# Kernel tuning notes

Hardware: AMD Instinct MI355X
Metric: run time of the kernel (lower is better)

Reference implementation:

```python
import jax, jax.numpy as jnp
import numpy as np

IN_FEATURES = 512
ACTION_DIM = 32
TRIL_DIM = ACTION_DIM * (ACTION_DIM + 1) // 2  # 528
BATCH = 65536
# Row-major lower-triangular indices; matches torch boolean-mask assignment order.
_ROWS, _COLS = np.tril_indices(ACTION_DIM)


def setup_inputs() -> dict:
    key = jax.random.key(0)
    k1, k2, k3, k4, k5 = jax.random.split(key, 5)
    logits = jax.random.normal(k1, (BATCH, IN_FEATURES), dtype=jnp.float32)
    best_action = jax.random.normal(k2, (BATCH, ACTION_DIM), dtype=jnp.float32)
    actions = jax.random.normal(k3, (BATCH, ACTION_DIM), dtype=jnp.float32)
    W = jax.random.normal(k4, (TRIL_DIM, IN_FEATURES), dtype=jnp.float32) * 0.02
    b = jax.random.normal(k5, (TRIL_DIM,), dtype=jnp.float32) * 0.02
    return {"logits": logits, "best_action": best_action, "actions": actions, "W": W, "b": b}


def reference(logits, best_action, actions, W, b):
    # Linear: [B, in_features] -> [B, tril_dim]
    flat_trils = logits @ W.T + b
    B = logits.shape[0]
    n = ACTION_DIM
    # Scatter flat vector into lower-triangular slots (row-major order).
    mats = jnp.zeros((B, n, n), dtype=flat_trils.dtype).at[:, _ROWS, _COLS].set(flat_trils)
    diag = jnp.eye(n, dtype=flat_trils.dtype)
    # Square the diagonal entries, keep off-diagonal entries as-is.
    tril = mats * mats * diag + (1.0 - diag) * mats
    action_diff = actions - best_action  # [B, n]
    vec = jnp.einsum('bij,bj->bi', tril, action_diff)  # [B, n]
    advantage = -0.5 * jnp.sum(vec * vec, axis=-1, keepdims=True)  # [B, 1]
    return advantage
```

## Files before the change

### kernel.cpp

```cpp
#include <hip/hip_runtime.h>
#include <hip/hip_bf16.h>


typedef __attribute__((ext_vector_type(8))) __bf16 bf16x8;
typedef __attribute__((ext_vector_type(4))) float f32x4;

#define AS1 __attribute__((address_space(1)))
#define AS3 __attribute__((address_space(3)))

__device__ __forceinline__ unsigned short f2b(float x) {
  unsigned u = __builtin_bit_cast(unsigned, x);
  u += 0x7fffu + ((u >> 16) & 1u);
  return (unsigned short)(u >> 16);
}
__device__ __forceinline__ float b2f(unsigned short h) {
  unsigned u = ((unsigned)h) << 16;
  return __builtin_bit_cast(float, u);
}

#define NFRAG 34
#define WK_BYTES (NFRAG * 1024)
#define AOFF (2 * WK_BYTES)
#define ABUF 4096
#define FL_STRIDE 1216
#define PL_OFF (64 * FL_STRIDE)
#define SMEM_BYTES (PL_OFF + 1024)

__global__ void prep_wp(const float* __restrict__ W, unsigned short* __restrict__ WP) {
  int t = blockIdx.x * 256 + threadIdx.x;
  int lane = t & 63;
  int u = t >> 6;
  int nf = u % NFRAG;
  int k16 = u / NFRAG;
  int n = nf * 16 + (lane & 15);
  int k0 = k16 * 32 + (lane >> 4) * 8;
  unsigned short h[8];
  if (n < 528) {
    const float* src = W + (size_t)n * 512 + k0;
#pragma unroll
    for (int j = 0; j < 8; ++j) h[j] = f2b(src[j]);
  } else {
#pragma unroll
    for (int j = 0; j < 8; ++j) h[j] = 0;
  }
  uint4 p;
  p.x = (unsigned)h[0] | ((unsigned)h[1] << 16);
  p.y = (unsigned)h[2] | ((unsigned)h[3] << 16);
  p.z = (unsigned)h[4] | ((unsigned)h[5] << 16);
  p.w = (unsigned)h[6] | ((unsigned)h[7] << 16);
  *(uint4*)(WP + (size_t)t * 8) = p;
}

template <int IT>
__device__ __forceinline__ float epi_partial(const char* smem,
                                             const float* __restrict__ actions,
                                             const float* __restrict__ best,
                                             int brow, int l) {
  float d[32];
  const float* ap = actions + (size_t)(brow + l) * 32;
  const float* bp = best + (size_t)(brow + l) * 32;
#pragma unroll
  for (int q = 0; q < 8; ++q) {
    float4 av = *(const float4*)(ap + q * 4);
    float4 bv = *(const float4*)(bp + q * 4);
    d[q * 4 + 0] = av.x - bv.x;
    d[q * 4 + 1] = av.y - bv.y;
    d[q * 4 + 2] = av.z - bv.z;
    d[q * 4 + 3] = av.w - bv.w;
  }
  const char* frow = smem + l * FL_STRIDE;
  const int swz = (l & 7) << 4;
  float ssum = 0.f;
#pragma unroll
  for (int ii = 0; ii < 8; ++ii) {
    const int i = IT + ii * 4;
    const int tri2 = i * (i + 1);
    const int s0 = tri2 >> 4;
    const int s1 = (tri2 + 2 * i) >> 4;
    float vec = 0.f;
#pragma unroll
    for (int s = s0; s <= s1; ++s) {
      uint4 w = *(const uint4*)(frow + ((s * 16) ^ swz));
      const unsigned* wp = (const unsigned*)&w;
#pragma unroll
      for (int e = 0; e < 8; ++e) {
        const int j = s * 8 + e - (tri2 >> 1);
        if (j < 0 || j > i) continue;
        unsigned short h = (e & 1) ? (unsigned short)(wp[e >> 1] >> 16)
                                   : (unsigned short)(wp[e >> 1] & 0xffffu);
        float v = b2f(h);
        if (j == i) vec += v * v * d[i];
        else        vec += v * d[j];
      }
    }
    ssum += vec * vec;
  }
  return ssum;
}

__global__ void __launch_bounds__(256, 2)
adv_kernel(const float* __restrict__ logits,
           const float* __restrict__ best,
           const float* __restrict__ actions,
           const float* __restrict__ bvec,
           const unsigned short* __restrict__ WP,
           float* __restrict__ out) {
  extern __shared__ char smem[];
  const int tid = threadIdx.x;
  const int l   = tid & 63;
  const int wid = tid >> 6;
  const int lr  = l & 15;
  const int lg  = l >> 4;
  const int start = wid * 8 + (wid > 0 ? 1 : 0);
  const int brow = blockIdx.x * 64;

  f32x4 acc[4][9];
  {
    f32x4 zero = {0.f, 0.f, 0.f, 0.f};
#pragma unroll
    for (int m = 0; m < 4; ++m)
#pragma unroll
      for (int n = 0; n < 9; ++n) acc[m][n] = zero;
  }

  const float* agbase = logits + (size_t)(brow + wid * 16 + lr) * 512 + lg * 8;

#define STAGE_W(dst, ks)                                                        \
  {                                                                             \
    const char* sW = (const char*)WP + (size_t)(ks) * WK_BYTES;                 \
    _Pragma("unroll")                                                           \
    for (int q = 0; q < 8; ++q) {                                               \
      int off = (q * 4 + wid) * 1024;                                           \
      __builtin_amdgcn_global_load_lds((AS1 unsigned int*)(sW + off + l * 16),  \
          (AS3 unsigned int*)((dst) + off), 16, 0, 0);                          \
    }                                                                           \
    if (wid < 2) {                                                              \
      int off = (32 + wid) * 1024;                                              \
      __builtin_amdgcn_global_load_lds((AS1 unsigned int*)(sW + off + l * 16),  \
          (AS3 unsigned int*)((dst) + off), 16, 0, 0);                          \
    }                                                                           \
  }

#define LOAD_A(dst, ks)                                                         \
  {                                                                             \
    const float* g = agbase + (ks) * 32;                                        \
    (dst)[0] = *(const float4*)(g);                                             \
    (dst)[1] = *(const float4*)(g + 4);                                         \
  }

#define WRITE_A(buf_idx, src)                                                   \
  {                                                                             \
    uint4 p;                                                                    \
    p.x = f2b((src)[0].x) | ((unsigned)f2b((src)[0].y) << 16);                  \
    p.y = f2b((src)[0].z) | ((unsigned)f2b((src)[0].w) << 16);                  \
    p.z = f2b((src)[1].x) | ((unsigned)f2b((src)[1].y) << 16);                  \
    p.w = f2b((src)[1].z) | ((unsigned)f2b((src)[1].w) << 16);                  \
    *(uint4*)(smem + AOFF + (buf_idx) * ABUF + tid * 16) = p;                   \
  }

#define COMPUTE(p)                                                              \
  {                                                                             \
    const char* ab = smem + AOFF + (p) * ABUF;                                  \
    const char* wb = smem + (p) * WK_BYTES;                                     \
    bf16x8 a[4];                                                                \
    _Pragma("unroll")                                                           \
    for (int m = 0; m < 4; ++m)                                                 \
      a[m] = *(const bf16x8*)(ab + m * 1024 + l * 16);                          \
    _Pragma("unroll")                                                           \
    for (int n = 0; n < 9; ++n) {                                               \
      bf16x8 w = *(const bf16x8*)(wb + (start + n) * 1024 + l * 16);            \
      _Pragma("unroll")                                                         \
      for (int m = 0; m < 4; ++m)                                               \
        acc[m][n] = __builtin_amdgcn_mfma_f32_16x16x32_bf16(a[m], w, acc[m][n], 0, 0, 0); \
    }                                                                           \
  }

  float4 pf0[2], pf1[2];
  LOAD_A(pf0, 0)
  LOAD_A(pf1, 1)
  STAGE_W(smem, 0)
  WRITE_A(0, pf0)
  __syncthreads();

  for (int t2 = 0; t2 < 16; t2 += 2) {
    if (t2 < 15) STAGE_W(smem + WK_BYTES, t2 + 1)
    if (t2 < 14) LOAD_A(pf0, t2 + 2)
    COMPUTE(0)
    if (t2 < 15) WRITE_A(1, pf1)
    __syncthreads();
    {
      int t = t2 + 1;
      if (t < 15) STAGE_W(smem, t + 1)
      if (t < 14) LOAD_A(pf1, t + 2)
      COMPUTE(1)
      if (t < 15) WRITE_A(0, pf0)
      __syncthreads();
    }
  }

#pragma unroll
  for (int n = 0; n < 9; ++n) {
    int nf = start + n;
    if (nf >= 33) continue;
    int f = nf * 16 + lr;
    float bb = bvec[f];
#pragma unroll
    for (int m = 0; m < 4; ++m)
#pragma unroll
      for (int r = 0; r < 4; ++r) {
        int row = m * 16 + lg * 4 + r;
        int byte = row * FL_STRIDE + ((f * 2) ^ ((row & 7) << 4));
        *(unsigned short*)(smem + byte) = f2b(acc[m][n][r] + bb);
      }
  }
  __syncthreads();

  float ssum;
  switch (wid) {
    case 0:  ssum = epi_partial<0>(smem, actions, best, brow, l); break;
    case 1:  ssum = epi_partial<1>(smem, actions, best, brow, l); break;
    case 2:  ssum = epi_partial<2>(smem, actions, best, brow, l); break;
    default: ssum = epi_partial<3>(smem, actions, best, brow, l); break;
  }
  ((float*)(smem + PL_OFF))[l * 4 + wid] = ssum;
  __syncthreads();
  if (tid < 64) {
    f32x4 p4 = *(const f32x4*)(smem + PL_OFF + tid * 16);
    out[brow + tid] = -0.5f * (p4[0] + p4[1] + p4[2] + p4[3]);
  }
}

extern "C" void kernel_launch(void* const* d_in, const int* in_sizes, int n_in,
                              void* d_out, int out_size, void* d_ws, size_t ws_size,
                              hipStream_t stream) {
  const float* logits  = (const float*)d_in[0];
  const float* best    = (const float*)d_in[1];
  const float* actions = (const float*)d_in[2];
  const float* W       = (const float*)d_in[3];
  const float* bvec    = (const float*)d_in[4];
  float* out = (float*)d_out;
  unsigned short* WP = (unsigned short*)d_ws;

  hipLaunchKernelGGL(prep_wp, dim3(136), dim3(256), 0, stream, W, WP);
  int M = in_sizes[0] / 512;
  hipLaunchKernelGGL(adv_kernel, dim3(M / 64), dim3(256), SMEM_BYTES, stream,
                     logits, best, actions, bvec, WP, out);
}
```

Before: 70.69 us.

## Replace syncthreads with partial vmcnt waits and raw barriers in GEMM pipeline

The main K-loop now uses explicit s_waitcnt with a partial vmcnt and raw s_barrier calls in place of __syncthreads. The intent is to let the next A-tile global loads stay in flight across the barrier while the LDS-direct W loads complete. The W staging is also made uniform: every wave issues 9 loads, and out-of-range slots are clamped to a padded LDS region. Sched barriers pin the order in which loads are issued. The manual vmcnt accounting is fragile: if the count of outstanding loads is wrong, the kernel can read LDS data before it has arrived.

```diff
diff --git a/kernel.cpp b/kernel.cpp
--- a/kernel.cpp
+++ b/kernel.cpp
@@ -20,11 +20,16 @@
 
 #define NFRAG 34
 #define WK_BYTES (NFRAG * 1024)
-#define AOFF (2 * WK_BYTES)
+#define WB_LDS 36864
+#define AOFF (2 * WB_LDS)
 #define ABUF 4096
 #define FL_STRIDE 1216
 #define PL_OFF (64 * FL_STRIDE)
-#define SMEM_BYTES (PL_OFF + 1024)
+#define SMEM_BYTES 81920
+
+#define SBAR0 __builtin_amdgcn_sched_barrier(0);
+#define WAITC(N) asm volatile("s_waitcnt vmcnt(" #N ") lgkmcnt(0)" ::: "memory");
+#define RAWBAR { SBAR0 __builtin_amdgcn_s_barrier(); SBAR0 }
 
 __global__ void prep_wp(const float* __restrict__ W, unsigned short* __restrict__ WP) {
   int t = blockIdx.x * 256 + threadIdx.x;
@@ -129,14 +134,10 @@
   {                                                                             \
     const char* sW = (const char*)WP + (size_t)(ks) * WK_BYTES;                 \
     _Pragma("unroll")                                                           \
-    for (int q = 0; q < 8; ++q) {                                               \
+    for (int q = 0; q < 9; ++q) {                                               \
       int off = (q * 4 + wid) * 1024;                                           \
-      __builtin_amdgcn_global_load_lds((AS1 unsigned int*)(sW + off + l * 16),  \
-          (AS3 unsigned int*)((dst) + off), 16, 0, 0);                          \
-    }                                                                           \
-    if (wid < 2) {                                                              \
-      int off = (32 + wid) * 1024;                                              \
-      __builtin_amdgcn_global_load_lds((AS1 unsigned int*)(sW + off + l * 16),  \
+      int soff = off < WK_BYTES ? off : (WK_BYTES - 1024);                      \
+      __builtin_amdgcn_global_load_lds((AS1 unsigned int*)(sW + soff + l * 16), \
           (AS3 unsigned int*)((dst) + off), 16, 0, 0);                          \
     }                                                                           \
   }
@@ -161,7 +162,7 @@
 #define COMPUTE(p)                                                              \
   {                                                                             \
     const char* ab = smem + AOFF + (p) * ABUF;                                  \
-    const char* wb = smem + (p) * WK_BYTES;                                     \
+    const char* wb = smem + (p) * WB_LDS;                                       \
     bf16x8 a[4];                                                                \
     _Pragma("unroll")                                                           \
     for (int m = 0; m < 4; ++m)                                                 \
@@ -176,27 +177,38 @@
   }
 
   float4 pf0[2], pf1[2];
+  STAGE_W(smem, 0)
+  SBAR0
   LOAD_A(pf0, 0)
   LOAD_A(pf1, 1)
-  STAGE_W(smem, 0)
+  SBAR0
   WRITE_A(0, pf0)
-  __syncthreads();
+  asm volatile("s_waitcnt lgkmcnt(0)" ::: "memory");
+  RAWBAR
 
   for (int t2 = 0; t2 < 16; t2 += 2) {
-    if (t2 < 15) STAGE_W(smem + WK_BYTES, t2 + 1)
+    if (t2 < 15) STAGE_W(smem + WB_LDS, t2 + 1)
+    SBAR0
     if (t2 < 14) LOAD_A(pf0, t2 + 2)
+    SBAR0
     COMPUTE(0)
     if (t2 < 15) WRITE_A(1, pf1)
-    __syncthreads();
+    if (t2 <= 12) { WAITC(2) }
+    else          { WAITC(0) }
+    RAWBAR
     {
-      int t = t2 + 1;
+      const int t = t2 + 1;
       if (t < 15) STAGE_W(smem, t + 1)
+      SBAR0
       if (t < 14) LOAD_A(pf1, t + 2)
+      SBAR0
       COMPUTE(1)
       if (t < 15) WRITE_A(0, pf0)
-      __syncthreads();
+      if (t <= 13) { WAITC(2) RAWBAR }
     }
   }
+  WAITC(0)
+  RAWBAR
 
 #pragma unroll
   for (int n = 0; n < 9; ++n) {
```

New measurement: 72.22 us. 2.2% more time.

## Load GEMM operands straight to registers and double the block to 128 rows

Applied to the files above, without the earlier changes.

The kernel stops staging W and A tiles in LDS with double buffering and barriers. Each wave now loads its own 9 W fragments and 4 A row-fragments from global memory into registers, converts A to bf16 in registers, and runs the MFMAs with raised scheduling priority. Blocks grow to 512 threads covering 128 rows, so two halves share the epilogue LDS. This removes LDS traffic and per-step syncs, but each wave now re-reads W from global/L2 instead of sharing it through LDS. The register prefetch only runs one step ahead, so latency hiding depends on occupancy.

```diff
diff --git a/kernel.cpp b/kernel.cpp
--- a/kernel.cpp
+++ b/kernel.cpp
@@ -4,9 +4,6 @@
 
 typedef __attribute__((ext_vector_type(8))) __bf16 bf16x8;
 typedef __attribute__((ext_vector_type(4))) float f32x4;
-
-#define AS1 __attribute__((address_space(1)))
-#define AS3 __attribute__((address_space(3)))
 
 __device__ __forceinline__ unsigned short f2b(float x) {
   unsigned u = __builtin_bit_cast(unsigned, x);
@@ -20,11 +17,9 @@
 
 #define NFRAG 34
 #define WK_BYTES (NFRAG * 1024)
-#define AOFF (2 * WK_BYTES)
-#define ABUF 4096
 #define FL_STRIDE 1216
-#define PL_OFF (64 * FL_STRIDE)
-#define SMEM_BYTES (PL_OFF + 1024)
+#define PL_OFF (128 * FL_STRIDE)
+#define SMEM_BYTES (PL_OFF + 2048)
 
 __global__ void prep_wp(const float* __restrict__ W, unsigned short* __restrict__ WP) {
   int t = blockIdx.x * 256 + threadIdx.x;
@@ -55,10 +50,10 @@
 __device__ __forceinline__ float epi_partial(const char* smem,
                                              const float* __restrict__ actions,
                                              const float* __restrict__ best,
-                                             int brow, int l) {
+                                             int growg, int lrow) {
   float d[32];
-  const float* ap = actions + (size_t)(brow + l) * 32;
-  const float* bp = best + (size_t)(brow + l) * 32;
+  const float* ap = actions + (size_t)growg * 32;
+  const float* bp = best + (size_t)growg * 32;
 #pragma unroll
   for (int q = 0; q < 8; ++q) {
     float4 av = *(const float4*)(ap + q * 4);
@@ -68,8 +63,8 @@
     d[q * 4 + 2] = av.z - bv.z;
     d[q * 4 + 3] = av.w - bv.w;
   }
-  const char* frow = smem + l * FL_STRIDE;
-  const int swz = (l & 7) << 4;
+  const char* frow = smem + lrow * FL_STRIDE;
+  const int swz = (lrow & 7) << 4;
   float ssum = 0.f;
 #pragma unroll
   for (int ii = 0; ii < 8; ++ii) {
@@ -98,7 +93,7 @@
   return ssum;
 }
 
-__global__ void __launch_bounds__(256, 2)
+__global__ void __launch_bounds__(512, 2)
 adv_kernel(const float* __restrict__ logits,
            const float* __restrict__ best,
            const float* __restrict__ actions,
@@ -106,13 +101,15 @@
            const unsigned short* __restrict__ WP,
            float* __restrict__ out) {
   extern __shared__ char smem[];
-  const int tid = threadIdx.x;
-  const int l   = tid & 63;
-  const int wid = tid >> 6;
-  const int lr  = l & 15;
-  const int lg  = l >> 4;
-  const int start = wid * 8 + (wid > 0 ? 1 : 0);
-  const int brow = blockIdx.x * 64;
+  const int tid  = threadIdx.x;
+  const int l    = tid & 63;
+  const int wid  = tid >> 6;
+  const int half = wid >> 2;
+  const int wc   = wid & 3;
+  const int lr   = l & 15;
+  const int lg   = l >> 4;
+  const int start = wc * 8 + (wc > 0 ? 1 : 0);
+  const int brow = blockIdx.x * 128;
 
   f32x4 acc[4][9];
   {
@@ -123,78 +120,59 @@
       for (int n = 0; n < 9; ++n) acc[m][n] = zero;
   }
 
-  const float* agbase = logits + (size_t)(brow + wid * 16 + lr) * 512 + lg * 8;
-
-#define STAGE_W(dst, ks)                                                        \
+  const char* wlane = (const char*)WP + (size_t)start * 1024 + (size_t)l * 16;
+  const float* ag0 = logits + (size_t)(brow + half * 64 + 0 * 16 + lr) * 512 + lg * 8;
+  const float* ag1 = logits + (size_t)(brow + half * 64 + 1 * 16 + lr) * 512 + lg * 8;
+  const float* ag2 = logits + (size_t)(brow + half * 64 + 2 * 16 + lr) * 512 + lg * 8;
+  const float* ag3 = logits + (size_t)(brow + half * 64 + 3 * 16 + lr) * 512 + lg * 8;
+
+  uint4 wreg[9];
+  float4 araw[4][2];
+
+#define LOADW(t)                                                                \
   {                                                                             \
-    const char* sW = (const char*)WP + (size_t)(ks) * WK_BYTES;                 \
+    const char* p = wlane + (size_t)(t) * WK_BYTES;                             \
     _Pragma("unroll")                                                           \
-    for (int q = 0; q < 8; ++q) {                                               \
-      int off = (q * 4 + wid) * 1024;                                           \
-      __builtin_amdgcn_global_load_lds((AS1 unsigned int*)(sW + off + l * 16),  \
-          (AS3 unsigned int*)((dst) + off), 16, 0, 0);                          \
-    }                                                                           \
-    if (wid < 2) {                                                              \
-      int off = (32 + wid) * 1024;                                              \
-      __builtin_amdgcn_global_load_lds((AS1 unsigned int*)(sW + off + l * 16),  \
-          (AS3 unsigned int*)((dst) + off), 16, 0, 0);                          \
-    }                                                                           \
-  }
-
-#define LOAD_A(dst, ks)                                                         \
+    for (int n = 0; n < 9; ++n) wreg[n] = *(const uint4*)(p + n * 1024);        \
+  }
+#define LOADA(t)                                                                \
   {                                                                             \
-    const float* g = agbase + (ks) * 32;                                        \
-    (dst)[0] = *(const float4*)(g);                                             \
-    (dst)[1] = *(const float4*)(g + 4);                                         \
-  }
-
-#define WRITE_A(buf_idx, src)                                                   \
-  {                                                                             \
-    uint4 p;                                                                    \
-    p.x = f2b((src)[0].x) | ((unsigned)f2b((src)[0].y) << 16);                  \
-    p.y = f2b((src)[0].z) | ((unsigned)f2b((src)[0].w) << 16);                  \
-    p.z = f2b((src)[1].x) | ((unsigned)f2b((src)[1].y) << 16);                  \
-    p.w = f2b((src)[1].z) | ((unsigned)f2b((src)[1].w) << 16);                  \
-    *(uint4*)(smem + AOFF + (buf_idx) * ABUF + tid * 16) = p;                   \
-  }
-
-#define COMPUTE(p)                                                              \
-  {                                                                             \
-    const char* ab = smem + AOFF + (p) * ABUF;                                  \
-    const char* wb = smem + (p) * WK_BYTES;                                     \
-    bf16x8 a[4];                                                                \
-    _Pragma("unroll")                                                           \
-    for (int m = 0; m < 4; ++m)                                                 \
-      a[m] = *(const bf16x8*)(ab + m * 1024 + l * 16);                          \
-    _Pragma("unroll")                                                           \
-    for (int n = 0; n < 9; ++n) {                                               \
-      bf16x8 w = *(const bf16x8*)(wb + (start + n) * 1024 + l * 16);            \
-      _Pragma("unroll")                                                         \
-      for (int m = 0; m < 4; ++m)                                               \
-        acc[m][n] = __builtin_amdgcn_mfma_f32_16x16x32_bf16(a[m], w, acc[m][n], 0, 0, 0); \
-    }                                                                           \
-  }
-
-  float4 pf0[2], pf1[2];
-  LOAD_A(pf0, 0)
-  LOAD_A(pf1, 1)
-  STAGE_W(smem, 0)
-  WRITE_A(0, pf0)
-  __syncthreads();
-
-  for (int t2 = 0; t2 < 16; t2 += 2) {
-    if (t2 < 15) STAGE_W(smem + WK_BYTES, t2 + 1)
-    if (t2 < 14) LOAD_A(pf0, t2 + 2)
-    COMPUTE(0)
-    if (t2 < 15) WRITE_A(1, pf1)
-    __syncthreads();
-    {
-      int t = t2 + 1;
-      if (t < 15) STAGE_W(smem, t + 1)
-      if (t < 14) LOAD_A(pf1, t + 2)
-      COMPUTE(1)
-      if (t < 15) WRITE_A(0, pf0)
-      __syncthreads();
+    araw[0][0] = *(const float4*)(ag0 + (t) * 32);                              \
+    araw[0][1] = *(const float4*)(ag0 + (t) * 32 + 4);                          \
+    araw[1][0] = *(const float4*)(ag1 + (t) * 32);                              \
+    araw[1][1] = *(const float4*)(ag1 + (t) * 32 + 4);                          \
+    araw[2][0] = *(const float4*)(ag2 + (t) * 32);                              \
+    araw[2][1] = *(const float4*)(ag2 + (t) * 32 + 4);                          \
+    araw[3][0] = *(const float4*)(ag3 + (t) * 32);                              \
+    araw[3][1] = *(const float4*)(ag3 + (t) * 32 + 4);                          \
+  }
+
+  LOADW(0)
+  LOADA(0)
+
+  for (int t = 0; t < 16; ++t) {
+    bf16x8 a[4];
+#pragma unroll
+    for (int m = 0; m < 4; ++m) {
+      bf16x8 af;
+      af[0] = (__bf16)araw[m][0].x; af[1] = (__bf16)araw[m][0].y;
+      af[2] = (__bf16)araw[m][0].z; af[3] = (__bf16)araw[m][0].w;
+      af[4] = (__bf16)araw[m][1].x; af[5] = (__bf16)araw[m][1].y;
+      af[6] = (__bf16)araw[m][1].z; af[7] = (__bf16)araw[m][1].w;
+      a[m] = af;
+    }
+    __builtin_amdgcn_s_setprio(1);
+#pragma unroll
+    for (int n = 0; n < 9; ++n) {
+      bf16x8 w = __builtin_bit_cast(bf16x8, wreg[n]);
+#pragma unroll
+      for (int m = 0; m < 4; ++m)
+        acc[m][n] = __builtin_amdgcn_mfma_f32_16x16x32_bf16(a[m], w, acc[m][n], 0, 0, 0);
+    }
+    __builtin_amdgcn_s_setprio(0);
+    if (t < 15) {
+      LOADW(t + 1)
+      LOADA(t + 1)
     }
   }
 
@@ -208,23 +186,27 @@
     for (int m = 0; m < 4; ++m)
 #pragma unroll
       for (int r = 0; r < 4; ++r) {
-        int row = m * 16 + lg * 4 + r;
+        int row = half * 64 + m * 16 + lg * 4 + r;
         int byte = row * FL_STRIDE + ((f * 2) ^ ((row & 7) << 4));
         *(unsigned short*)(smem + byte) = f2b(acc[m][n][r] + bb);
       }
   }
   __syncthreads();
 
-  float ssum;
-  switch (wid) {
-    case 0:  ssum = epi_partial<0>(smem, actions, best, brow, l); break;
-    case 1:  ssum = epi_partial<1>(smem, actions, best, brow, l); break;
-    case 2:  ssum = epi_partial<2>(smem, actions, best, brow, l); break;
-    default: ssum = epi_partial<3>(smem, actions, best, brow, l); break;
-  }
-  ((float*)(smem + PL_OFF))[l * 4 + wid] = ssum;
+  {
+    const int lrow = half * 64 + l;
+    const int growg = brow + lrow;
+    float ssum;
+    switch (wc) {
+      case 0:  ssum = epi_partial<0>(smem, actions, best, growg, lrow); break;
+      case 1:  ssum = epi_partial<1>(smem, actions, best, growg, lrow); break;
+      case 2:  ssum = epi_partial<2>(smem, actions, best, growg, lrow); break;
+      default: ssum = epi_partial<3>(smem, actions, best, growg, lrow); break;
+    }
+    ((float*)(smem + PL_OFF))[lrow * 4 + wc] = ssum;
+  }
   __syncthreads();
-  if (tid < 64) {
+  if (tid < 128) {
     f32x4 p4 = *(const f32x4*)(smem + PL_OFF + tid * 16);
     out[brow + tid] = -0.5f * (p4[0] + p4[1] + p4[2] + p4[3]);
   }
@@ -243,6 +225,6 @@
 
   hipLaunchKernelGGL(prep_wp, dim3(136), dim3(256), 0, stream, W, WP);
   int M = in_sizes[0] / 512;
-  hipLaunchKernelGGL(adv_kernel, dim3(M / 64), dim3(256), SMEM_BYTES, stream,
+  hipLaunchKernelGGL(adv_kernel, dim3(M / 128), dim3(512), SMEM_BYTES, stream,
                      logits, best, actions, bvec, WP, out);
 }
```

Result: slower. 98.08 us (+38.8%).

## Split output columns across two blocks per row tile and reduce partial vectors separately

Applied to the files above, without the earlier changes.

Each 64-row tile is now handled by two blocks, each computing half of the 528 output columns. This halves the per-block W staging and accumulator footprint, which lets occupancy rise from two to three blocks per CU. The logits are now read straight from global memory into registers inside the compute step and converted to bf16, replacing the LDS A staging. Each block writes partial triangular matrix-vector products to a workspace, and a new reduce kernel combines the two halves and computes the squared sum. The cost is that logits are read twice, there is extra workspace traffic, and an additional kernel launch.

```diff
diff --git a/kernel.cpp b/kernel.cpp
--- a/kernel.cpp
+++ b/kernel.cpp
@@ -20,11 +20,10 @@
 
 #define NFRAG 34
 #define WK_BYTES (NFRAG * 1024)
-#define AOFF (2 * WK_BYTES)
-#define ABUF 4096
-#define FL_STRIDE 1216
-#define PL_OFF (64 * FL_STRIDE)
-#define SMEM_BYTES (PL_OFF + 1024)
+#define WSTEP 17408
+#define FL2_STRIDE 640
+#define SMEM_BYTES 40960
+#define WS2_OFF 557056
 
 __global__ void prep_wp(const float* __restrict__ W, unsigned short* __restrict__ WP) {
   int t = blockIdx.x * 256 + threadIdx.x;
@@ -51,14 +50,14 @@
   *(uint4*)(WP + (size_t)t * 8) = p;
 }
 
-template <int IT>
-__device__ __forceinline__ float epi_partial(const char* smem,
+template <int IT, int LO>
+__device__ __forceinline__ void epi_partial2(const char* smem,
                                              const float* __restrict__ actions,
                                              const float* __restrict__ best,
-                                             int brow, int l) {
+                                             int grow, int lrow, float* pv) {
   float d[32];
-  const float* ap = actions + (size_t)(brow + l) * 32;
-  const float* bp = best + (size_t)(brow + l) * 32;
+  const float* ap = actions + (size_t)grow * 32;
+  const float* bp = best + (size_t)grow * 32;
 #pragma unroll
   for (int q = 0; q < 8; ++q) {
     float4 av = *(const float4*)(ap + q * 4);
@@ -68,166 +67,188 @@
     d[q * 4 + 2] = av.z - bv.z;
     d[q * 4 + 3] = av.w - bv.w;
   }
-  const char* frow = smem + l * FL_STRIDE;
-  const int swz = (l & 7) << 4;
-  float ssum = 0.f;
+  const char* frow = smem + lrow * FL2_STRIDE;
+  const int swz = (lrow & 7) << 4;
 #pragma unroll
   for (int ii = 0; ii < 8; ++ii) {
     const int i = IT + ii * 4;
-    const int tri2 = i * (i + 1);
-    const int s0 = tri2 >> 4;
-    const int s1 = (tri2 + 2 * i) >> 4;
+    const int tri = (i * (i + 1)) >> 1;
+    const int jlo = (LO > tri) ? (LO - tri) : 0;
+    const int jhi = (i < LO + 271 - tri) ? i : (LO + 271 - tri);
     float vec = 0.f;
-#pragma unroll
-    for (int s = s0; s <= s1; ++s) {
-      uint4 w = *(const uint4*)(frow + ((s * 16) ^ swz));
-      const unsigned* wp = (const unsigned*)&w;
-#pragma unroll
-      for (int e = 0; e < 8; ++e) {
-        const int j = s * 8 + e - (tri2 >> 1);
-        if (j < 0 || j > i) continue;
-        unsigned short h = (e & 1) ? (unsigned short)(wp[e >> 1] >> 16)
-                                   : (unsigned short)(wp[e >> 1] & 0xffffu);
-        float v = b2f(h);
-        if (j == i) vec += v * v * d[i];
-        else        vec += v * d[j];
+    if (jlo <= jhi) {
+      const int s0 = ((tri + jlo - LO) * 2) >> 4;
+      const int s1 = ((tri + jhi - LO) * 2) >> 4;
+#pragma unroll
+      for (int s = s0; s <= s1; ++s) {
+        uint4 w = *(const uint4*)(frow + ((s * 16) ^ swz));
+        const unsigned* wp = (const unsigned*)&w;
+#pragma unroll
+        for (int e = 0; e < 8; ++e) {
+          const int j = s * 8 + e + LO - tri;
+          if (j < jlo || j > jhi) continue;
+          unsigned short h = (e & 1) ? (unsigned short)(wp[e >> 1] >> 16)
+                                     : (unsigned short)(wp[e >> 1] & 0xffffu);
+          float v = b2f(h);
+          if (j == i) vec += v * v * d[i];
+          else        vec += v * d[j];
+        }
       }
     }
-    ssum += vec * vec;
-  }
-  return ssum;
-}
-
-__global__ void __launch_bounds__(256, 2)
+    pv[ii] = vec;
+  }
+}
+
+__global__ void __launch_bounds__(256, 3)
 adv_kernel(const float* __restrict__ logits,
            const float* __restrict__ best,
            const float* __restrict__ actions,
            const float* __restrict__ bvec,
            const unsigned short* __restrict__ WP,
-           float* __restrict__ out) {
+           float* __restrict__ ws2) {
   extern __shared__ char smem[];
   const int tid = threadIdx.x;
   const int l   = tid & 63;
   const int wid = tid >> 6;
   const int lr  = l & 15;
   const int lg  = l >> 4;
-  const int start = wid * 8 + (wid > 0 ? 1 : 0);
-  const int brow = blockIdx.x * 64;
-
-  f32x4 acc[4][9];
+  const int c      = blockIdx.x & 1;
+  const int brow   = (blockIdx.x >> 1) * 64;
+  const int cstart = c * 17;
+  const int startr = wid * 4;
+
+  f32x4 acc[4][5];
   {
     f32x4 zero = {0.f, 0.f, 0.f, 0.f};
 #pragma unroll
     for (int m = 0; m < 4; ++m)
 #pragma unroll
-      for (int n = 0; n < 9; ++n) acc[m][n] = zero;
-  }
-
-  const float* agbase = logits + (size_t)(brow + wid * 16 + lr) * 512 + lg * 8;
+      for (int n = 0; n < 5; ++n) acc[m][n] = zero;
+  }
 
 #define STAGE_W(dst, ks)                                                        \
   {                                                                             \
-    const char* sW = (const char*)WP + (size_t)(ks) * WK_BYTES;                 \
-    _Pragma("unroll")                                                           \
-    for (int q = 0; q < 8; ++q) {                                               \
-      int off = (q * 4 + wid) * 1024;                                           \
-      __builtin_amdgcn_global_load_lds((AS1 unsigned int*)(sW + off + l * 16),  \
-          (AS3 unsigned int*)((dst) + off), 16, 0, 0);                          \
-    }                                                                           \
-    if (wid < 2) {                                                              \
-      int off = (32 + wid) * 1024;                                              \
-      __builtin_amdgcn_global_load_lds((AS1 unsigned int*)(sW + off + l * 16),  \
-          (AS3 unsigned int*)((dst) + off), 16, 0, 0);                          \
-    }                                                                           \
-  }
-
-#define LOAD_A(dst, ks)                                                         \
+    const char* sW = (const char*)WP + (size_t)(ks) * WK_BYTES +                \
+                     (size_t)cstart * 1024;                                     \
+    _Pragma("unroll")                                                           \
+    for (int q = 0; q < 4; ++q) {                                               \
+      int fr = wid + q * 4;                                                     \
+      __builtin_amdgcn_global_load_lds(                                         \
+          (AS1 unsigned int*)(sW + fr * 1024 + l * 16),                         \
+          (AS3 unsigned int*)((dst) + fr * 1024 + l * 16), 16, 0, 0);           \
+    }                                                                           \
+    if (wid == 0)                                                               \
+      __builtin_amdgcn_global_load_lds(                                         \
+          (AS1 unsigned int*)(sW + 16 * 1024 + l * 16),                         \
+          (AS3 unsigned int*)((dst) + 16 * 1024 + l * 16), 16, 0, 0);           \
+  }
+
+#define COMPUTE(p, t)                                                           \
   {                                                                             \
-    const float* g = agbase + (ks) * 32;                                        \
-    (dst)[0] = *(const float4*)(g);                                             \
-    (dst)[1] = *(const float4*)(g + 4);                                         \
-  }
-
-#define WRITE_A(buf_idx, src)                                                   \
-  {                                                                             \
-    uint4 p;                                                                    \
-    p.x = f2b((src)[0].x) | ((unsigned)f2b((src)[0].y) << 16);                  \
-    p.y = f2b((src)[0].z) | ((unsigned)f2b((src)[0].w) << 16);                  \
-    p.z = f2b((src)[1].x) | ((unsigned)f2b((src)[1].y) << 16);                  \
-    p.w = f2b((src)[1].z) | ((unsigned)f2b((src)[1].w) << 16);                  \
-    *(uint4*)(smem + AOFF + (buf_idx) * ABUF + tid * 16) = p;                   \
-  }
-
-#define COMPUTE(p)                                                              \
-  {                                                                             \
-    const char* ab = smem + AOFF + (p) * ABUF;                                  \
-    const char* wb = smem + (p) * WK_BYTES;                                     \
+    const char* wb = smem + (p) * WSTEP;                                        \
+    f32x4 x[4][2];                                                              \
+    _Pragma("unroll")                                                           \
+    for (int m = 0; m < 4; ++m) {                                               \
+      const float* g = logits + (size_t)(brow + m * 16 + lr) * 512 +            \
+                       (t) * 32 + lg * 8;                                       \
+      x[m][0] = *(const f32x4*)(g);                                             \
+      x[m][1] = *(const f32x4*)(g + 4);                                         \
+    }                                                                           \
     bf16x8 a[4];                                                                \
     _Pragma("unroll")                                                           \
-    for (int m = 0; m < 4; ++m)                                                 \
-      a[m] = *(const bf16x8*)(ab + m * 1024 + l * 16);                          \
-    _Pragma("unroll")                                                           \
-    for (int n = 0; n < 9; ++n) {                                               \
-      bf16x8 w = *(const bf16x8*)(wb + (start + n) * 1024 + l * 16);            \
+    for (int m = 0; m < 4; ++m) {                                               \
+      bf16x8 af;                                                                \
+      af[0] = (__bf16)x[m][0][0]; af[1] = (__bf16)x[m][0][1];                   \
+      af[2] = (__bf16)x[m][0][2]; af[3] = (__bf16)x[m][0][3];                   \
+      af[4] = (__bf16)x[m][1][0]; af[5] = (__bf16)x[m][1][1];                   \
+      af[6] = (__bf16)x[m][1][2]; af[7] = (__bf16)x[m][1][3];                   \
+      a[m] = af;                                                                \
+    }                                                                           \
+    _Pragma("unroll")                                                           \
+    for (int n = 0; n < 5; ++n) {                                               \
+      bf16x8 w = *(const bf16x8*)(wb + (startr + n) * 1024 + l * 16);           \
       _Pragma("unroll")                                                         \
       for (int m = 0; m < 4; ++m)                                               \
         acc[m][n] = __builtin_amdgcn_mfma_f32_16x16x32_bf16(a[m], w, acc[m][n], 0, 0, 0); \
     }                                                                           \
   }
 
-  float4 pf0[2], pf1[2];
-  LOAD_A(pf0, 0)
-  LOAD_A(pf1, 1)
   STAGE_W(smem, 0)
-  WRITE_A(0, pf0)
   __syncthreads();
 
   for (int t2 = 0; t2 < 16; t2 += 2) {
-    if (t2 < 15) STAGE_W(smem + WK_BYTES, t2 + 1)
-    if (t2 < 14) LOAD_A(pf0, t2 + 2)
-    COMPUTE(0)
-    if (t2 < 15) WRITE_A(1, pf1)
+    if (t2 < 15) STAGE_W(smem + WSTEP, t2 + 1)
+    COMPUTE(0, t2)
     __syncthreads();
-    {
-      int t = t2 + 1;
-      if (t < 15) STAGE_W(smem, t + 1)
-      if (t < 14) LOAD_A(pf1, t + 2)
-      COMPUTE(1)
-      if (t < 15) WRITE_A(0, pf0)
-      __syncthreads();
+    if (t2 + 2 < 16) STAGE_W(smem, t2 + 2)
+    COMPUTE(1, t2 + 1)
+    __syncthreads();
+  }
+
+#pragma unroll
+  for (int n = 0; n < 5; ++n) {
+    int f_rel = (startr + n) * 16 + lr;
+    int f_abs = c * 272 + f_rel;
+    if (f_abs < 528) {
+      float bb = bvec[f_abs];
+#pragma unroll
+      for (int m = 0; m < 4; ++m)
+#pragma unroll
+        for (int r = 0; r < 4; ++r) {
+          int row = m * 16 + lg * 4 + r;
+          int byte = row * FL2_STRIDE + ((f_rel * 2) ^ ((row & 7) << 4));
+          *(unsigned short*)(smem + byte) = f2b(acc[m][n][r] + bb);
+        }
     }
   }
-
-#pragma unroll
-  for (int n = 0; n < 9; ++n) {
-    int nf = start + n;
-    if (nf >= 33) continue;
-    int f = nf * 16 + lr;
-    float bb = bvec[f];
-#pragma unroll
-    for (int m = 0; m < 4; ++m)
-#pragma unroll
-      for (int r = 0; r < 4; ++r) {
-        int row = m * 16 + lg * 4 + r;
-        int byte = row * FL_STRIDE + ((f * 2) ^ ((row & 7) << 4));
-        *(unsigned short*)(smem + byte) = f2b(acc[m][n][r] + bb);
+  __syncthreads();
+
+  {
+    int it  = tid & 3;
+    int lrow = tid >> 2;
+    int grow = brow + lrow;
+    float pv[8];
+    if (c == 0) {
+      switch (it) {
+        case 0:  epi_partial2<0, 0>(smem, actions, best, grow, lrow, pv); break;
+        case 1:  epi_partial2<1, 0>(smem, actions, best, grow, lrow, pv); break;
+        case 2:  epi_partial2<2, 0>(smem, actions, best, grow, lrow, pv); break;
+        default: epi_partial2<3, 0>(smem, actions, best, grow, lrow, pv); break;
       }
-  }
-  __syncthreads();
-
-  float ssum;
-  switch (wid) {
-    case 0:  ssum = epi_partial<0>(smem, actions, best, brow, l); break;
-    case 1:  ssum = epi_partial<1>(smem, actions, best, brow, l); break;
-    case 2:  ssum = epi_partial<2>(smem, actions, best, brow, l); break;
-    default: ssum = epi_partial<3>(smem, actions, best, brow, l); break;
-  }
-  ((float*)(smem + PL_OFF))[l * 4 + wid] = ssum;
-  __syncthreads();
-  if (tid < 64) {
-    f32x4 p4 = *(const f32x4*)(smem + PL_OFF + tid * 16);
-    out[brow + tid] = -0.5f * (p4[0] + p4[1] + p4[2] + p4[3]);
-  }
+    } else {
+      switch (it) {
+        case 0:  epi_partial2<0, 272>(smem, actions, best, grow, lrow, pv); break;
+        case 1:  epi_partial2<1, 272>(smem, actions, best, grow, lrow, pv); break;
+        case 2:  epi_partial2<2, 272>(smem, actions, best, grow, lrow, pv); break;
+        default: epi_partial2<3, 272>(smem, actions, best, grow, lrow, pv); break;
+      }
+    }
+    float* wsp = ws2 + (size_t)grow * 64 + c * 32 + it * 8;
+    float4 v0 = {pv[0], pv[1], pv[2], pv[3]};
+    float4 v1 = {pv[4], pv[5], pv[6], pv[7]};
+    *(float4*)(wsp)     = v0;
+    *(float4*)(wsp + 4) = v1;
+  }
+}
+
+__global__ void __launch_bounds__(256)
+reduce_k(const float* __restrict__ ws2, float* __restrict__ out) {
+  int row = blockIdx.x * 256 + threadIdx.x;
+  const float* p = ws2 + (size_t)row * 64;
+  float v[64];
+#pragma unroll
+  for (int q = 0; q < 16; ++q) {
+    float4 x = *(const float4*)(p + q * 4);
+    v[q * 4 + 0] = x.x; v[q * 4 + 1] = x.y; v[q * 4 + 2] = x.z; v[q * 4 + 3] = x.w;
+  }
+  float ssum = 0.f;
+#pragma unroll
+  for (int i = 0; i < 32; ++i) {
+    int it = i & 3, ii = i >> 2;
+    float vec = v[it * 8 + ii] + v[32 + it * 8 + ii];
+    ssum += vec * vec;
+  }
+  out[row] = -0.5f * ssum;
 }
 
 extern "C" void kernel_launch(void* const* d_in, const int* in_sizes, int n_in,
@@ -240,9 +261,11 @@
   const float* bvec    = (const float*)d_in[4];
   float* out = (float*)d_out;
   unsigned short* WP = (unsigned short*)d_ws;
+  float* ws2 = (float*)((char*)d_ws + WS2_OFF);
 
   hipLaunchKernelGGL(prep_wp, dim3(136), dim3(256), 0, stream, W, WP);
   int M = in_sizes[0] / 512;
-  hipLaunchKernelGGL(adv_kernel, dim3(M / 64), dim3(256), SMEM_BYTES, stream,
-                     logits, best, actions, bvec, WP, out);
-}
+  hipLaunchKernelGGL(adv_kernel, dim3((M / 64) * 2), dim3(256), SMEM_BYTES,
+                     stream, logits, best, actions, bvec, WP, ws2);
+  hipLaunchKernelGGL(reduce_k, dim3(M / 256), dim3(256), 0, stream, ws2, out);
+}
```

New measurement: 169.3 us. 2.4x slower.
